# Kernel optimization log

Measured on AMD Instinct MI355X. Metric: run time of the kernel, lower is better.

The kernel has to match this reference:

```python
import jax, jax.numpy as jnp
import numpy as np

B, N, HID = 4, 1024, 256
NH, DH = 8, 32          # heads, head dim (HID = NH*DH)
BH = 64                 # bias MLP hidden


def setup_inputs() -> dict:
    key = jax.random.key(0)
    ks = jax.random.split(key, 12)
    s = lambda fan_in: 1.0 / np.sqrt(fan_in)
    return {
        "h": jax.random.normal(ks[0], (B, N, HID), jnp.float32),
        "coord": jax.random.uniform(ks[1], (B, N), jnp.float32),
        "mask": jnp.ones((B, N), jnp.int32),
        # qkv / proj linear params (stored [in, out])
        "Wqkv": jax.random.normal(ks[2], (HID, 3 * HID), jnp.float32) * s(HID),
        "bqkv": jnp.zeros((3 * HID,), jnp.float32),
        "Wproj": jax.random.normal(ks[3], (HID, HID), jnp.float32) * s(HID),
        "bproj": jnp.zeros((HID,), jnp.float32),
        # layernorm
        "gamma": jnp.ones((HID,), jnp.float32),
        "beta": jnp.zeros((HID,), jnp.float32),
        # relative-bias MLP: Linear(1->BH), SiLU, Linear(BH->BH), SiLU, Linear(BH->NH)
        "Wb1": jax.random.normal(ks[4], (1, BH), jnp.float32),
        "bb1": jnp.zeros((BH,), jnp.float32),
        "Wb2": jax.random.normal(ks[5], (BH, BH), jnp.float32) * s(BH),
        "bb2": jnp.zeros((BH,), jnp.float32),
        "Wb3": jax.random.normal(ks[6], (BH, NH), jnp.float32) * s(BH),
        "bb3": jnp.zeros((NH,), jnp.float32),
    }


def _layernorm(x, gamma, beta, eps=1e-5):
    mu = jnp.mean(x, axis=-1, keepdims=True)
    var = jnp.mean((x - mu) ** 2, axis=-1, keepdims=True)
    return (x - mu) * jax.lax.rsqrt(var + eps) * gamma + beta


def reference(h, coord, mask, Wqkv, bqkv, Wproj, bproj, gamma, beta,
              Wb1, bb1, Wb2, bb2, Wb3, bb3):
    x = _layernorm(h, gamma, beta)                      # [B,N,HID]
    qkv = x @ Wqkv + bqkv                               # [B,N,3*HID]
    q, k, v = jnp.split(qkv, 3, axis=-1)
    # [B,N,HID] -> [B,NH,N,DH]
    reshape = lambda t: t.reshape(B, N, NH, DH).transpose(0, 2, 1, 3)
    q, k, v = reshape(q), reshape(k), reshape(v)

    attn = jnp.einsum("bhqd,bhkd->bhqk", q, k) / np.sqrt(DH).astype(np.float32)

    # pairwise coordinate differences and learned bias
    dcoord = coord[:, None, :] - coord[:, :, None]      # [B,N,N]
    t = dcoord[..., None]                               # [B,N,N,1]
    t = jax.nn.silu(t @ Wb1 + bb1)                      # [B,N,N,BH]
    t = jax.nn.silu(t @ Wb2 + bb2)                      # [B,N,N,BH]
    bias = (t @ Wb3 + bb3)                              # [B,N,N,NH]
    attn = attn + bias.transpose(0, 3, 1, 2)            # [B,NH,N,N]

    neg_inf = jnp.array(-jnp.inf, attn.dtype)
    attn = jnp.where(mask[:, None, None, :] == 0, neg_inf, attn)
    w = jax.nn.softmax(attn, axis=-1)

    out = jnp.einsum("bhqk,bhkd->bhqd", w, v)           # [B,NH,N,DH]
    out = out.transpose(0, 2, 1, 3).reshape(B, N, HID)
    out = out @ Wproj + bproj
    return h + out
```

## Files before the change

kernel.cpp:

```cpp
#include <hip/hip_runtime.h>
#include <hip/hip_fp16.h>
#include <math.h>

#define BB   4
#define NN   1024
#define HIDD 256
#define NHD  8
#define DHD  32
#define BHD  64
#define TI2  2048
#define LOG2E 1.4426950408889634f

typedef __attribute__((ext_vector_type(8))) short bf16x8;
typedef __attribute__((ext_vector_type(4))) short bf16x4;
typedef __attribute__((ext_vector_type(4))) float f32x4;

__device__ __forceinline__ unsigned short f2bf(float x) {
  union { float f; unsigned u; } c; c.f = x;
  unsigned r = c.u + 0x7FFFu + ((c.u >> 16) & 1u);
  return (unsigned short)(r >> 16);
}
__device__ __forceinline__ float bf2f(unsigned short b) {
  union { unsigned u; float f; } c; c.u = ((unsigned)b) << 16;
  return c.f;
}

__device__ __forceinline__ void pv_mfma(f32x4& acc, bf16x4 a, bf16x4 b) {
#if __has_builtin(__builtin_amdgcn_mfma_f32_16x16x16bf16_1k)
  acc = __builtin_amdgcn_mfma_f32_16x16x16bf16_1k(a, b, acc, 0, 0, 0);
#else
  asm volatile("s_nop 1\n\t"
               "v_mfma_f32_16x16x16_bf16 %0, %1, %2, %0\n\t"
               "s_nop 7\n\t"
               "s_nop 3"
               : "+v"(acc) : "v"(a), "v"(b));
#endif
}

__global__ __launch_bounds__(256) void prep_kernel(
    const float* __restrict__ Wb1, const float* __restrict__ bb1,
    const float* __restrict__ Wb2, const float* __restrict__ bb2,
    const float* __restrict__ Wb3, const float* __restrict__ bb3,
    const float* __restrict__ Wqkv, const float* __restrict__ Wproj,
    unsigned* __restrict__ tblh, unsigned short* __restrict__ wtq,
    unsigned short* __restrict__ wtp)
{
  __shared__ float h1a[4][64], h1b[4][64], h2a[4][64], h2b[4][64];
  __shared__ float t[16][17];
  int bid = blockIdx.x, tid = threadIdx.x;
  if (bid < 512) {
    int g = tid >> 6, j = tid & 63;
    int pt = bid * 4 + g;
    float t0 = -1.0f + (float)pt     * (2.0f / (float)TI2);
    float t1 = -1.0f + (float)(pt+1) * (2.0f / (float)TI2);
    float w1 = Wb1[j], c1 = bb1[j];
    float z0 = fmaf(t0, w1, c1), z1 = fmaf(t1, w1, c1);
    h1a[g][j] = z0 / (1.0f + __expf(-z0));
    h1b[g][j] = z1 / (1.0f + __expf(-z1));
    __syncthreads();
    float a0 = bb2[j], a1 = a0;
    #pragma unroll 16
    for (int i = 0; i < BHD; ++i) {
      float wv = Wb2[i*BHD + j];
      a0 = fmaf(h1a[g][i], wv, a0);
      a1 = fmaf(h1b[g][i], wv, a1);
    }
    h2a[g][j] = a0 / (1.0f + __expf(-a0));
    h2b[g][j] = a1 / (1.0f + __expf(-a1));
    __syncthreads();
    if (j < NHD) {
      float o0 = bb3[j], o1 = o0;
      #pragma unroll 16
      for (int i = 0; i < BHD; ++i) {
        float wv = Wb3[i*NHD + j];
        o0 = fmaf(h2a[g][i], wv, o0);
        o1 = fmaf(h2b[g][i], wv, o1);
      }
      o0 *= LOG2E; o1 *= LOG2E;
      __half2 hh = __floats2half2_rn(o0, o1 - o0);
      tblh[j*TI2 + pt] = *(unsigned*)&hh;
    }
  } else {
    const float* W; unsigned short* Wt; int n0, k0, ncols;
    if (bid < 1280) {
      int rb = bid - 512;
      n0 = (rb % 48) * 16; k0 = (rb / 48) * 16; ncols = 768;
      W = Wqkv; Wt = wtq;
    } else {
      int rc = bid - 1280;
      n0 = (rc & 15) * 16; k0 = (rc >> 4) * 16; ncols = 256;
      W = Wproj; Wt = wtp;
    }
    int sx = tid & 15, sy = tid >> 4;
    t[sy][sx] = W[(size_t)(k0 + sy) * ncols + n0 + sx];
    __syncthreads();
    Wt[(size_t)(n0 + sy) * 256 + k0 + sx] = f2bf(t[sx][sy]);
  }
}

__global__ __launch_bounds__(256) void ln_qkv_mm_kernel(
    const float* __restrict__ h, const float* __restrict__ gamma,
    const float* __restrict__ beta, const unsigned short* __restrict__ Wt,
    const float* __restrict__ bqkv,
    unsigned short* __restrict__ qws, unsigned short* __restrict__ kws,
    unsigned short* __restrict__ vtws)
{
  __shared__ unsigned short xs[64][260];
  int tid = threadIdx.x;
  int m0 = blockIdx.x * 64, n0 = blockIdx.y * 128;

  {
    int r = tid >> 2, q = tid & 3;
    const float* hrow = h + (size_t)(m0 + r)*HIDD + q*64;
    float4 xv[16];
    float sum = 0.f, sq = 0.f;
    #pragma unroll
    for (int j = 0; j < 16; ++j) {
      xv[j] = *(const float4*)&hrow[j*4];
      sum += xv[j].x + xv[j].y + xv[j].z + xv[j].w;
      sq  += xv[j].x*xv[j].x + xv[j].y*xv[j].y + xv[j].z*xv[j].z + xv[j].w*xv[j].w;
    }
    sum += __shfl_xor(sum, 1); sq += __shfl_xor(sq, 1);
    sum += __shfl_xor(sum, 2); sq += __shfl_xor(sq, 2);
    float mu  = sum * (1.0f/HIDD);
    float var = sq  * (1.0f/HIDD) - mu*mu;
    float rs  = rsqrtf(var + 1e-5f);
    #pragma unroll
    for (int j2 = 0; j2 < 8; ++j2) {
      union { bf16x8 v; unsigned short u[8]; } o;
      #pragma unroll
      for (int e = 0; e < 2; ++e) {
        float4 x4 = xv[j2*2 + e];
        int col = q*64 + j2*8 + e*4;
        float4 gv = *(const float4*)&gamma[col];
        float4 bv = *(const float4*)&beta[col];
        o.u[e*4+0] = f2bf(fmaf((x4.x - mu)*rs, gv.x, bv.x));
        o.u[e*4+1] = f2bf(fmaf((x4.y - mu)*rs, gv.y, bv.y));
        o.u[e*4+2] = f2bf(fmaf((x4.z - mu)*rs, gv.z, bv.z));
        o.u[e*4+3] = f2bf(fmaf((x4.w - mu)*rs, gv.w, bv.w));
      }
      *(bf16x8*)&xs[r][q*64 + j2*8] = o.v;
    }
  }
  __syncthreads();

  int lane = tid & 63, w = tid >> 6;
  int lo = lane & 15, hi = lane >> 4;
  int m0w = m0 + w*16;
  f32x4 acc[8];
  #pragma unroll
  for (int nt = 0; nt < 8; ++nt) acc[nt] = (f32x4){0.f,0.f,0.f,0.f};

  #pragma unroll
  for (int ks = 0; ks < 8; ++ks) {
    bf16x8 af = *(const bf16x8*)&xs[w*16 + lo][ks*32 + hi*8];
    #pragma unroll
    for (int nt = 0; nt < 8; ++nt) {
      bf16x8 bf = *(const bf16x8*)&Wt[(size_t)(n0 + nt*16 + lo)*256 + ks*32 + hi*8];
      acc[nt] = __builtin_amdgcn_mfma_f32_16x16x32_bf16(af, bf, acc[nt], 0, 0, 0);
    }
  }

  int b = m0w >> 10;
  if (n0 < 512) {
    unsigned short* dst = (n0 < 256) ? qws : kws;
    int nbase = (m0w & 1023) + hi*4;
    #pragma unroll
    for (int nt = 0; nt < 8; ++nt) {
      int c = n0 + nt*16 + lo;
      int cr = c & 255;
      int head = cr >> 5, d = cr & 31;
      float bq = bqkv[c];
      size_t bh = (size_t)(b*NHD + head);
      #pragma unroll
      for (int r = 0; r < 4; ++r)
        dst[(bh*NN + nbase + r)*DHD + d] = f2bf(acc[nt][r] + bq);
    }
  } else {
    __syncthreads();
    unsigned short (*vt)[72] = (unsigned short(*)[72])&xs[0][0];
    #pragma unroll
    for (int nt = 0; nt < 8; ++nt) {
      int cr = nt*16 + lo;
      float bq = bqkv[n0 + cr];
      union { unsigned short u[4]; unsigned wd[2]; } pk;
      #pragma unroll
      for (int r = 0; r < 4; ++r) pk.u[r] = f2bf(acc[nt][r] + bq);
      int col = w*16 + hi*4;
      *(unsigned*)&vt[cr][col]     = pk.wd[0];
      *(unsigned*)&vt[cr][col + 2] = pk.wd[1];
    }
    __syncthreads();
    int nn0 = m0 & 1023;
    #pragma unroll
    for (int i = 0; i < 4; ++i) {
      int u = i*256 + tid;
      int row = u >> 3, ch = u & 7;
      int cr256 = (n0 - 512) + row;
      int head = cr256 >> 5, d = cr256 & 31;
      *(bf16x8*)&vtws[((size_t)(b*NHD + head)*DHD + d)*NN + nn0 + ch*8] =
          *(const bf16x8*)&vt[row][ch*8];
    }
  }
}

__global__ __launch_bounds__(256, 4) void attn_kernel(
    const unsigned short* __restrict__ Q, const unsigned short* __restrict__ K,
    const unsigned short* __restrict__ Vt, const float* __restrict__ coord,
    const int* __restrict__ mask, const unsigned* __restrict__ tblh,
    unsigned short* __restrict__ pO, float2* __restrict__ pML)
{
  __shared__ unsigned tableL[TI2];
  __shared__ unsigned short Klds[2][64][40];
  __shared__ unsigned short Vtlds[2][32][72];

  int tid = threadIdx.x, lane = tid & 63, w = tid >> 6;
  int bh = blockIdx.y, half = blockIdx.z;
  int b = bh >> 3, head = bh & 7;
  int qbase = blockIdx.x * 64 + w * 16;
  int lo = lane & 15, hi = lane >> 4;

  for (int i = tid; i < TI2/4; i += 256)
    ((uint4*)tableL)[i] = ((const uint4*)(tblh + head*TI2))[i];

  bf16x8 qf = *(const bf16x8*)&Q[((size_t)bh*NN + qbase + lo)*DHD + hi*8];
  float qoff = fmaf(coord[b*NN + qbase + lo], -(float)TI2*0.5f, (float)TI2*0.5f);

  float m = -1e30f, l = 0.f;
  f32x4 oacc[2];
  oacc[0] = (f32x4){0.f,0.f,0.f,0.f};
  oacc[1] = (f32x4){0.f,0.f,0.f,0.f};
  const float scale2 = 0.17677669529663689f * LOG2E;

  int kt0 = half * (NN/2);
  int sr = tid >> 2, ss = tid & 3;
  int vr = tid >> 3, vs = tid & 7;
  {
    *(bf16x8*)&Klds[0][sr][ss*8] =
        *(const bf16x8*)&K[((size_t)bh*NN + kt0 + sr)*DHD + ss*8];
    *(bf16x8*)&Vtlds[0][vr][vs*8] =
        *(const bf16x8*)&Vt[((size_t)bh*DHD + vr)*NN + kt0 + vs*8];
  }
  __syncthreads();

  for (int t = 0; t < 8; ++t) {
    int kt = kt0 + t*64;
    int cur = t & 1;
    bf16x8 kn, vn;
    if (t < 7) {
      kn = *(const bf16x8*)&K[((size_t)bh*NN + kt + 64 + sr)*DHD + ss*8];
      vn = *(const bf16x8*)&Vt[((size_t)bh*DHD + vr)*NN + kt + 64 + vs*8];
    }
    float ck[4][4]; int mk[4][4];
    #pragma unroll
    for (int nt = 0; nt < 4; ++nt) {
      float4 c4 = *(const float4*)&coord[b*NN + kt + nt*16 + hi*4];
      int4   m4 = *(const int4*)  &mask [b*NN + kt + nt*16 + hi*4];
      ck[nt][0] = c4.x; ck[nt][1] = c4.y; ck[nt][2] = c4.z; ck[nt][3] = c4.w;
      mk[nt][0] = m4.x; mk[nt][1] = m4.y; mk[nt][2] = m4.z; mk[nt][3] = m4.w;
    }

    f32x4 z = {0.f,0.f,0.f,0.f};
    f32x4 sacc[4];
    #pragma unroll
    for (int nt = 0; nt < 4; ++nt) {
      bf16x8 kf = *(const bf16x8*)&Klds[cur][nt*16 + lo][hi*8];
      sacc[nt] = __builtin_amdgcn_mfma_f32_16x16x32_bf16(kf, qf, z, 0, 0, 0);
    }

    float sv[4][4];
    #pragma unroll
    for (int nt = 0; nt < 4; ++nt) {
      #pragma unroll
      for (int r = 0; r < 4; ++r) {
        float u = fmaf(ck[nt][r], (float)TI2*0.5f, qoff);
        u = fminf(fmaxf(u, 0.0f), (float)TI2 - 0.01f);
        int   i0 = (int)u;
        float fr = u - (float)i0;
        unsigned e = tableL[i0];
        __half2 hh = *(__half2*)&e;
        float bias = fmaf(__high2float(hh), fr, __low2float(hh));
        float s = fmaf(sacc[nt][r], scale2, bias);
        sv[nt][r] = mk[nt][r] ? s : -1e31f;
      }
    }

    float pm = sv[0][0];
    #pragma unroll
    for (int nt = 0; nt < 4; ++nt)
      #pragma unroll
      for (int r = 0; r < 4; ++r) pm = fmaxf(pm, sv[nt][r]);
    pm = fmaxf(pm, __shfl_xor(pm, 16));
    pm = fmaxf(pm, __shfl_xor(pm, 32));
    float mn = fmaxf(m, pm);
    if (mn > m) {
      float sf = __builtin_amdgcn_exp2f(m - mn);
      l *= sf;
      #pragma unroll
      for (int n2 = 0; n2 < 2; ++n2)
        #pragma unroll
        for (int r = 0; r < 4; ++r) oacc[n2][r] *= sf;
      m = mn;
    }

    bf16x4 pfrag[4];
    #pragma unroll
    for (int nt = 0; nt < 4; ++nt) {
      float p0 = __builtin_amdgcn_exp2f(sv[nt][0] - m);
      float p1 = __builtin_amdgcn_exp2f(sv[nt][1] - m);
      float p2 = __builtin_amdgcn_exp2f(sv[nt][2] - m);
      float p3 = __builtin_amdgcn_exp2f(sv[nt][3] - m);
      l += (p0 + p1) + (p2 + p3);
      union { bf16x4 v; unsigned short u[4]; } pk;
      pk.u[0] = f2bf(p0); pk.u[1] = f2bf(p1);
      pk.u[2] = f2bf(p2); pk.u[3] = f2bf(p3);
      pfrag[nt] = pk.v;
    }

    #pragma unroll
    for (int nt = 0; nt < 4; ++nt) {
      #pragma unroll
      for (int n2 = 0; n2 < 2; ++n2) {
        bf16x4 vf = *(const bf16x4*)&Vtlds[cur][n2*16 + lo][nt*16 + hi*4];
        pv_mfma(oacc[n2], vf, pfrag[nt]);
      }
    }

    if (t < 7) {
      *(bf16x8*)&Klds[cur^1][sr][ss*8] = kn;
      *(bf16x8*)&Vtlds[cur^1][vr][vs*8] = vn;
    }
    __syncthreads();
  }

  l += __shfl_xor(l, 16);
  l += __shfl_xor(l, 32);
  size_t base = ((size_t)(half*BB*NHD + bh)*NN + qbase + lo);
  #pragma unroll
  for (int n2 = 0; n2 < 2; ++n2) {
    union { bf16x4 v; unsigned short u[4]; } ov;
    ov.u[0] = f2bf(oacc[n2][0]); ov.u[1] = f2bf(oacc[n2][1]);
    ov.u[2] = f2bf(oacc[n2][2]); ov.u[3] = f2bf(oacc[n2][3]);
    *(bf16x4*)&pO[base*DHD + n2*16 + hi*4] = ov.v;
  }
  if (hi == 0) pML[base] = make_float2(m, l);
}

__global__ __launch_bounds__(128) void proj_mm_kernel(
    const unsigned short* __restrict__ pO, const float2* __restrict__ pML,
    const unsigned short* __restrict__ Wpt, const float* __restrict__ bp,
    const float* __restrict__ h, float* __restrict__ out)
{
  __shared__ unsigned short alds[32][264];
  int tid = threadIdx.x;
  int m0 = blockIdx.x * 32, n0 = blockIdx.y * 64;

  {
    int r = tid >> 2, q = tid & 3;
    int g = m0 + r, b = g >> 10, n = g & 1023;
    #pragma unroll
    for (int hh = 0; hh < 2; ++hh) {
      int hd = q*2 + hh;
      int bhh = b*NHD + hd;
      float2 ml0 = pML[(size_t)bhh*NN + n];
      float2 ml1 = pML[((size_t)(BB*NHD) + bhh)*NN + n];
      float mm = fmaxf(ml0.x, ml1.x);
      float e0 = __builtin_amdgcn_exp2f(ml0.x - mm);
      float e1 = __builtin_amdgcn_exp2f(ml1.x - mm);
      float inv = 1.0f / fmaf(ml0.y, e0, ml1.y * e1);
      e0 *= inv; e1 *= inv;
      const bf16x8* p0 = (const bf16x8*)&pO[((size_t)bhh*NN + n)*DHD];
      const bf16x8* p1 = (const bf16x8*)&pO[(((size_t)(BB*NHD) + bhh)*NN + n)*DHD];
      #pragma unroll
      for (int j = 0; j < 4; ++j) {
        union { bf16x8 v; unsigned short u[8]; } a, c, o;
        a.v = p0[j]; c.v = p1[j];
        #pragma unroll
        for (int e = 0; e < 8; ++e)
          o.u[e] = f2bf(fmaf(bf2f(a.u[e]), e0, bf2f(c.u[e]) * e1));
        *(bf16x8*)&alds[r][hd*32 + j*8] = o.v;
      }
    }
  }
  __syncthreads();

  int lane = tid & 63, w = tid >> 6;
  int lo = lane & 15, hi = lane >> 4;
  f32x4 acc[4];
  #pragma unroll
  for (int nt = 0; nt < 4; ++nt) acc[nt] = (f32x4){0.f,0.f,0.f,0.f};

  #pragma unroll
  for (int ks = 0; ks < 8; ++ks) {
    bf16x8 af = *(const bf16x8*)&alds[w*16 + lo][ks*32 + hi*8];
    #pragma unroll
    for (int nt = 0; nt < 4; ++nt) {
      bf16x8 bf = *(const bf16x8*)&Wpt[(size_t)(n0 + nt*16 + lo)*256 + ks*32 + hi*8];
      acc[nt] = __builtin_amdgcn_mfma_f32_16x16x32_bf16(af, bf, acc[nt], 0, 0, 0);
    }
  }

  int m0w = m0 + w*16;
  #pragma unroll
  for (int nt = 0; nt < 4; ++nt) {
    int c = n0 + nt*16 + lo;
    float bpv = bp[c];
    #pragma unroll
    for (int r = 0; r < 4; ++r) {
      size_t o = (size_t)(m0w + hi*4 + r)*HIDD + c;
      out[o] = h[o] + acc[nt][r] + bpv;
    }
  }
}

extern "C" void kernel_launch(void* const* d_in, const int* in_sizes, int n_in,
                              void* d_out, int out_size, void* d_ws, size_t ws_size,
                              hipStream_t stream)
{
  const float* h     = (const float*)d_in[0];
  const float* coord = (const float*)d_in[1];
  const int*   mask  = (const int*)  d_in[2];
  const float* Wqkv  = (const float*)d_in[3];
  const float* bqkv  = (const float*)d_in[4];
  const float* Wproj = (const float*)d_in[5];
  const float* bproj = (const float*)d_in[6];
  const float* gamma = (const float*)d_in[7];
  const float* beta  = (const float*)d_in[8];
  const float* Wb1   = (const float*)d_in[9];
  const float* bb1   = (const float*)d_in[10];
  const float* Wb2   = (const float*)d_in[11];
  const float* bb2   = (const float*)d_in[12];
  const float* Wb3   = (const float*)d_in[13];
  const float* bb3   = (const float*)d_in[14];
  float* out = (float*)d_out;

  unsigned* tblh = (unsigned*)d_ws;
  float2*   pML  = (float2*)(tblh + NHD*TI2);
  unsigned short* wtq  = (unsigned short*)(pML + (size_t)2*BB*NHD*NN);
  unsigned short* wtp  = wtq + 768*256;
  unsigned short* qws  = wtp + 256*256;
  unsigned short* kws  = qws + (size_t)BB*NHD*NN*DHD;
  unsigned short* vtws = kws + (size_t)BB*NHD*NN*DHD;
  unsigned short* pO   = vtws + (size_t)BB*NHD*NN*DHD;

  prep_kernel<<<dim3(1536), dim3(256), 0, stream>>>(
      Wb1, bb1, Wb2, bb2, Wb3, bb3, Wqkv, Wproj, tblh, wtq, wtp);
  ln_qkv_mm_kernel<<<dim3(BB*NN/64, 6), dim3(256), 0, stream>>>(
      h, gamma, beta, wtq, bqkv, qws, kws, vtws);
  attn_kernel<<<dim3(NN/64, BB*NHD, 2), dim3(256), 0, stream>>>(
      qws, kws, vtws, coord, mask, tblh, pO, pML);
  proj_mm_kernel<<<dim3(BB*NN/32, 4), dim3(128), 0, stream>>>(
      pO, pML, wtp, bproj, h, out);
}
```

Before: 73.58 us.

## Drop split-K attention, normalize in-kernel and simplify projection GEMM

The attention kernel no longer splits the key range across two blocks. Each block now walks all 16 key tiles, normalizes its output by the row sum, and writes bf16 straight into a [B,N,HID] activation buffer. The projection kernel drops the LSE merge of the two partial outputs and reads A fragments directly from global memory with 256-thread blocks. This removes the partial-result traffic and the merge work, but halves the number of attention blocks (512 instead of 1024) and doubles each block's serial loop length, which may reduce latency hiding.

```diff
diff --git a/kernel.cpp b/kernel.cpp
--- a/kernel.cpp
+++ b/kernel.cpp
@@ -208,14 +208,14 @@
     const unsigned short* __restrict__ Q, const unsigned short* __restrict__ K,
     const unsigned short* __restrict__ Vt, const float* __restrict__ coord,
     const int* __restrict__ mask, const unsigned* __restrict__ tblh,
-    unsigned short* __restrict__ pO, float2* __restrict__ pML)
+    unsigned short* __restrict__ ao)
 {
   __shared__ unsigned tableL[TI2];
   __shared__ unsigned short Klds[2][64][40];
   __shared__ unsigned short Vtlds[2][32][72];
 
   int tid = threadIdx.x, lane = tid & 63, w = tid >> 6;
-  int bh = blockIdx.y, half = blockIdx.z;
+  int bh = blockIdx.y;
   int b = bh >> 3, head = bh & 7;
   int qbase = blockIdx.x * 64 + w * 16;
   int lo = lane & 15, hi = lane >> 4;
@@ -232,22 +232,21 @@
   oacc[1] = (f32x4){0.f,0.f,0.f,0.f};
   const float scale2 = 0.17677669529663689f * LOG2E;
 
-  int kt0 = half * (NN/2);
   int sr = tid >> 2, ss = tid & 3;
   int vr = tid >> 3, vs = tid & 7;
   {
     *(bf16x8*)&Klds[0][sr][ss*8] =
-        *(const bf16x8*)&K[((size_t)bh*NN + kt0 + sr)*DHD + ss*8];
+        *(const bf16x8*)&K[((size_t)bh*NN + sr)*DHD + ss*8];
     *(bf16x8*)&Vtlds[0][vr][vs*8] =
-        *(const bf16x8*)&Vt[((size_t)bh*DHD + vr)*NN + kt0 + vs*8];
+        *(const bf16x8*)&Vt[((size_t)bh*DHD + vr)*NN + vs*8];
   }
   __syncthreads();
 
-  for (int t = 0; t < 8; ++t) {
-    int kt = kt0 + t*64;
+  for (int t = 0; t < 16; ++t) {
+    int kt = t*64;
     int cur = t & 1;
     bf16x8 kn, vn;
-    if (t < 7) {
+    if (t < 15) {
       kn = *(const bf16x8*)&K[((size_t)bh*NN + kt + 64 + sr)*DHD + ss*8];
       vn = *(const bf16x8*)&Vt[((size_t)bh*DHD + vr)*NN + kt + 64 + vs*8];
     }
@@ -326,7 +325,7 @@
       }
     }
 
-    if (t < 7) {
+    if (t < 15) {
       *(bf16x8*)&Klds[cur^1][sr][ss*8] = kn;
       *(bf16x8*)&Vtlds[cur^1][vr][vs*8] = vn;
     }
@@ -335,64 +334,33 @@
 
   l += __shfl_xor(l, 16);
   l += __shfl_xor(l, 32);
-  size_t base = ((size_t)(half*BB*NHD + bh)*NN + qbase + lo);
+  float inv = 1.0f / l;
+  size_t obase = ((size_t)(b*NN + qbase + lo))*HIDD + head*DHD;
   #pragma unroll
   for (int n2 = 0; n2 < 2; ++n2) {
     union { bf16x4 v; unsigned short u[4]; } ov;
-    ov.u[0] = f2bf(oacc[n2][0]); ov.u[1] = f2bf(oacc[n2][1]);
-    ov.u[2] = f2bf(oacc[n2][2]); ov.u[3] = f2bf(oacc[n2][3]);
-    *(bf16x4*)&pO[base*DHD + n2*16 + hi*4] = ov.v;
-  }
-  if (hi == 0) pML[base] = make_float2(m, l);
-}
-
-__global__ __launch_bounds__(128) void proj_mm_kernel(
-    const unsigned short* __restrict__ pO, const float2* __restrict__ pML,
-    const unsigned short* __restrict__ Wpt, const float* __restrict__ bp,
-    const float* __restrict__ h, float* __restrict__ out)
+    ov.u[0] = f2bf(oacc[n2][0] * inv); ov.u[1] = f2bf(oacc[n2][1] * inv);
+    ov.u[2] = f2bf(oacc[n2][2] * inv); ov.u[3] = f2bf(oacc[n2][3] * inv);
+    *(bf16x4*)&ao[obase + n2*16 + hi*4] = ov.v;
+  }
+}
+
+__global__ __launch_bounds__(256) void proj_mm_kernel(
+    const unsigned short* __restrict__ AO, const unsigned short* __restrict__ Wpt,
+    const float* __restrict__ bp, const float* __restrict__ h,
+    float* __restrict__ out)
 {
-  __shared__ unsigned short alds[32][264];
-  int tid = threadIdx.x;
-  int m0 = blockIdx.x * 32, n0 = blockIdx.y * 64;
-
-  {
-    int r = tid >> 2, q = tid & 3;
-    int g = m0 + r, b = g >> 10, n = g & 1023;
-    #pragma unroll
-    for (int hh = 0; hh < 2; ++hh) {
-      int hd = q*2 + hh;
-      int bhh = b*NHD + hd;
-      float2 ml0 = pML[(size_t)bhh*NN + n];
-      float2 ml1 = pML[((size_t)(BB*NHD) + bhh)*NN + n];
-      float mm = fmaxf(ml0.x, ml1.x);
-      float e0 = __builtin_amdgcn_exp2f(ml0.x - mm);
-      float e1 = __builtin_amdgcn_exp2f(ml1.x - mm);
-      float inv = 1.0f / fmaf(ml0.y, e0, ml1.y * e1);
-      e0 *= inv; e1 *= inv;
-      const bf16x8* p0 = (const bf16x8*)&pO[((size_t)bhh*NN + n)*DHD];
-      const bf16x8* p1 = (const bf16x8*)&pO[(((size_t)(BB*NHD) + bhh)*NN + n)*DHD];
-      #pragma unroll
-      for (int j = 0; j < 4; ++j) {
-        union { bf16x8 v; unsigned short u[8]; } a, c, o;
-        a.v = p0[j]; c.v = p1[j];
-        #pragma unroll
-        for (int e = 0; e < 8; ++e)
-          o.u[e] = f2bf(fmaf(bf2f(a.u[e]), e0, bf2f(c.u[e]) * e1));
-        *(bf16x8*)&alds[r][hd*32 + j*8] = o.v;
-      }
-    }
-  }
-  __syncthreads();
-
-  int lane = tid & 63, w = tid >> 6;
+  int tid = threadIdx.x, lane = tid & 63, w = tid >> 6;
   int lo = lane & 15, hi = lane >> 4;
+  int m0 = blockIdx.x * 64 + w * 16;
+  int n0 = blockIdx.y * 64;
   f32x4 acc[4];
   #pragma unroll
   for (int nt = 0; nt < 4; ++nt) acc[nt] = (f32x4){0.f,0.f,0.f,0.f};
 
   #pragma unroll
   for (int ks = 0; ks < 8; ++ks) {
-    bf16x8 af = *(const bf16x8*)&alds[w*16 + lo][ks*32 + hi*8];
+    bf16x8 af = *(const bf16x8*)&AO[(size_t)(m0 + lo)*256 + ks*32 + hi*8];
     #pragma unroll
     for (int nt = 0; nt < 4; ++nt) {
       bf16x8 bf = *(const bf16x8*)&Wpt[(size_t)(n0 + nt*16 + lo)*256 + ks*32 + hi*8];
@@ -400,14 +368,13 @@
     }
   }
 
-  int m0w = m0 + w*16;
   #pragma unroll
   for (int nt = 0; nt < 4; ++nt) {
     int c = n0 + nt*16 + lo;
     float bpv = bp[c];
     #pragma unroll
     for (int r = 0; r < 4; ++r) {
-      size_t o = (size_t)(m0w + hi*4 + r)*HIDD + c;
+      size_t o = (size_t)(m0 + hi*4 + r)*HIDD + c;
       out[o] = h[o] + acc[nt][r] + bpv;
     }
   }
@@ -435,20 +402,19 @@
   float* out = (float*)d_out;
 
   unsigned* tblh = (unsigned*)d_ws;
-  float2*   pML  = (float2*)(tblh + NHD*TI2);
-  unsigned short* wtq  = (unsigned short*)(pML + (size_t)2*BB*NHD*NN);
+  unsigned short* wtq  = (unsigned short*)(tblh + NHD*TI2);
   unsigned short* wtp  = wtq + 768*256;
   unsigned short* qws  = wtp + 256*256;
   unsigned short* kws  = qws + (size_t)BB*NHD*NN*DHD;
   unsigned short* vtws = kws + (size_t)BB*NHD*NN*DHD;
-  unsigned short* pO   = vtws + (size_t)BB*NHD*NN*DHD;
+  unsigned short* aob  = vtws + (size_t)BB*NHD*NN*DHD;
 
   prep_kernel<<<dim3(1536), dim3(256), 0, stream>>>(
       Wb1, bb1, Wb2, bb2, Wb3, bb3, Wqkv, Wproj, tblh, wtq, wtp);
   ln_qkv_mm_kernel<<<dim3(BB*NN/64, 6), dim3(256), 0, stream>>>(
       h, gamma, beta, wtq, bqkv, qws, kws, vtws);
-  attn_kernel<<<dim3(NN/64, BB*NHD, 2), dim3(256), 0, stream>>>(
-      qws, kws, vtws, coord, mask, tblh, pO, pML);
-  proj_mm_kernel<<<dim3(BB*NN/32, 4), dim3(128), 0, stream>>>(
-      pO, pML, wtp, bproj, h, out);
-}
+  attn_kernel<<<dim3(NN/64, BB*NHD), dim3(256), 0, stream>>>(
+      qws, kws, vtws, coord, mask, tblh, aob);
+  proj_mm_kernel<<<dim3(BB*NN/64, 4), dim3(256), 0, stream>>>(
+      aob, wtp, bproj, h, out);
+}
```

After: 80.44 us. 1.09x slower.
